# Performance work log

Hardware: AMD Instinct MI355X
Metric: run time of the kernel (lower is better)

Reference implementation:

```python
import jax, jax.numpy as jnp
import numpy as np

N_NODES = 100000
N_EDGES = 1600000
DIM = 64
BN_EPS = 1e-5


def setup_inputs() -> dict:
    key = jax.random.key(0)
    ks = jax.random.split(key, 6)
    x = jax.random.normal(ks[0], (N_NODES, DIM), dtype=jnp.float32)
    edge_index = jax.random.randint(ks[1], (2, N_EDGES), 0, N_NODES, dtype=jnp.int32)
    W = jax.random.normal(ks[2], (DIM, DIM), dtype=jnp.float32) / np.sqrt(DIM)
    b = jax.random.normal(ks[3], (DIM,), dtype=jnp.float32) * 0.01
    gamma = jnp.ones((DIM,), dtype=jnp.float32)
    beta = jnp.zeros((DIM,), dtype=jnp.float32)
    return {"x": x, "edge_index": edge_index, "W": W, "b": b, "gamma": gamma, "beta": beta}


def reference(x, edge_index, W, b, gamma, beta):
    n = x.shape[0]
    src, dst = edge_index[0], edge_index[1]
    # GCNConv adds self loops
    loop = jnp.arange(n, dtype=edge_index.dtype)
    src = jnp.concatenate([src, loop])
    dst = jnp.concatenate([dst, loop])
    # symmetric degree normalization: D^-1/2 (A+I) D^-1/2
    deg = jax.ops.segment_sum(jnp.ones(src.shape[0], x.dtype), dst, num_segments=n)
    dinv = jnp.where(deg > 0, jax.lax.rsqrt(deg), 0.0)
    norm = dinv[src] * dinv[dst]  # [E+N]
    h = x @ W  # [N, D] transform before aggregation (GCN order)
    msg = h[src] * norm[:, None]  # gather + scale
    out = jax.ops.segment_sum(msg, dst, num_segments=n) + b  # scatter-add
    # BatchNorm1d (training mode: batch statistics, biased variance)
    mean = jnp.mean(out, axis=0)
    var = jnp.mean(jnp.square(out - mean), axis=0)
    out = (out - mean) * jax.lax.rsqrt(var + BN_EPS) * gamma + beta
    # ReLU; dropout is identity in eval mode
    return jax.nn.relu(out)
```

## Files before the change

kernel.cpp:

```cpp
#include <hip/hip_runtime.h>

#define N_NODES 100000
#define N_EDGES 1600000
#define DIM 64
#define BN_EPS 1e-5f

#define BNODES 128
#define NBUCK ((N_NODES + BNODES - 1) / BNODES)
#define CAP_RAW 2560
#define CAP_OUT 3584
#define TILE 4096
#define ABLK ((N_EDGES + TILE - 1) / TILE)

#define GBLK 6250
#define NREP 32

typedef __bf16 bf16x8 __attribute__((ext_vector_type(8)));
typedef float floatx4 __attribute__((ext_vector_type(4)));

static __device__ __forceinline__ unsigned short f2bf(float f) {
    unsigned u = __float_as_uint(f);
    u = (u + 0x7FFFu + ((u >> 16) & 1u)) >> 16;
    return (unsigned short)u;
}
static __device__ __forceinline__ float bf2f(unsigned short h) {
    return __uint_as_float(((unsigned)h) << 16);
}

__global__ void __launch_bounds__(1024)
passA_kernel(const int* __restrict__ src, const int* __restrict__ dst,
             int* __restrict__ cur, unsigned int* __restrict__ entries, int E) {
    __shared__ int hist[NBUCK];
    __shared__ int lbase[NBUCK];
    int t = threadIdx.x;
    if (t < NBUCK) hist[t] = 0;
    __syncthreads();

    int e0   = blockIdx.x * TILE;
    int eend = min(e0 + TILE, E);
    int eb   = e0 + t * 4;

    int dreg[4], sreg[4], ne = 0;
    if (eb + 3 < eend) {
        int4 d4 = *(const int4*)(dst + eb);
        int4 s4 = *(const int4*)(src + eb);
        dreg[0] = d4.x; dreg[1] = d4.y; dreg[2] = d4.z; dreg[3] = d4.w;
        sreg[0] = s4.x; sreg[1] = s4.y; sreg[2] = s4.z; sreg[3] = s4.w;
        ne = 4;
    } else {
        for (int e = eb; e < eend && ne < 4; ++e, ++ne) {
            dreg[ne] = dst[e];
            sreg[ne] = src[e];
        }
    }
#pragma unroll
    for (int k = 0; k < 4; ++k)
        if (k < ne) atomicAdd(&hist[dreg[k] >> 7], 1);
    __syncthreads();
    if (t < NBUCK) {
        int ii = t + (blockIdx.x * 331) % NBUCK;
        if (ii >= NBUCK) ii -= NBUCK;
        int c = hist[ii];
        lbase[ii] = (c > 0) ? atomicAdd(&cur[ii], c) : 0;
        hist[ii] = 0;
    }
    __syncthreads();
#pragma unroll
    for (int k = 0; k < 4; ++k) {
        if (k >= ne) break;
        int s = sreg[k];
        int d = dreg[k];
        int b = d >> 7;
        int r = atomicAdd(&hist[b], 1);
        int pos = lbase[b] + r;
        if (pos < CAP_RAW)
            entries[(size_t)b * CAP_OUT + pos] = ((unsigned)s << 7) | (unsigned)(d & 127);
    }
}

__global__ void __launch_bounds__(256)
build_kernel(unsigned int* __restrict__ entries, const int* __restrict__ cur,
             int* __restrict__ rowbeg, int* __restrict__ rowend,
             float* __restrict__ dinv,
             const float* __restrict__ x, const float* __restrict__ W,
             unsigned short* __restrict__ hb, int dummyIdx, int N) {
    __shared__ int hist[BNODES * 4];
    __shared__ int nstart[BNODES];
    __shared__ int cursor[BNODES * 4];
    __shared__ float sdinv[BNODES];
    __shared__ int w0tot;
    int bucket = blockIdx.x;
    int t = threadIdx.x;
    int lane = t & 63, wv = t >> 6;
    int node0 = bucket * BNODES;
    int nn = min(BNODES, N - node0);
    int cnt = min(cur[bucket], CAP_RAW);
    unsigned int* eb = entries + (size_t)bucket * CAP_OUT;

    for (int i = t; i < BNODES * 4; i += 256) hist[i] = 0;
    __syncthreads();

    unsigned int ereg[10];
#pragma unroll
    for (int k = 0; k < 10; ++k) {
        int i = t + k * 256;
        if (i < cnt) {
            unsigned int e = eb[i];
            ereg[k] = e;
            int s = (int)(e >> 7);
            int q = (s >= 25000) + (s >= 50000) + (s >= 75000);
            atomicAdd(&hist[((e & 127) << 2) | q], 1);
        }
    }
    __syncthreads();

    int deg_t = 0, pdeg_t = 0;
    if (t < BNODES) {
        deg_t = hist[t * 4] + hist[t * 4 + 1] + hist[t * 4 + 2] + hist[t * 4 + 3];
        pdeg_t = (deg_t + 7) & ~7;
    }
    int v = pdeg_t;
#pragma unroll
    for (int off = 1; off < 64; off <<= 1) {
        int u = __shfl_up(v, off, 64);
        if (lane >= off) v += u;
    }
    if (t == 63) w0tot = v;
    __syncthreads();
    if (t < BNODES) {
        int incl = v + (wv == 1 ? w0tot : 0);
        int ex = incl - pdeg_t;
        nstart[t] = ex;
        int o = ex;
        cursor[t * 4 + 0] = o; o += hist[t * 4 + 0];
        cursor[t * 4 + 1] = o; o += hist[t * 4 + 1];
        cursor[t * 4 + 2] = o; o += hist[t * 4 + 2];
        cursor[t * 4 + 3] = o;
    }
    __syncthreads();
#pragma unroll
    for (int k = 0; k < 10; ++k) {
        int i = t + k * 256;
        if (i < cnt) {
            unsigned int e = ereg[k];
            int s = (int)(e >> 7);
            int q = (s >= 25000) + (s >= 50000) + (s >= 75000);
            int p = atomicAdd(&cursor[((e & 127) << 2) | q], 1);
            eb[p] = (unsigned)s;
        }
    }
    if (t < nn) {
        int dg  = deg_t;
        int pdg = pdeg_t;
        int base = nstart[t];
        for (int k = dg; k < pdg; ++k) eb[base + k] = (unsigned)dummyIdx;
        int gbase = bucket * CAP_OUT + base;
        rowbeg[node0 + t] = gbase;
        rowend[node0 + t] = gbase + pdg;
        float di = rsqrtf((float)(dg + 1));
        dinv[node0 + t] = di;
        sdinv[t] = di;
    }
    __syncthreads();

    int m = lane & 15, quad = lane >> 4;
    int nchunk = nn >> 4;
    bf16x8 bfrag[2][4];
#pragma unroll
    for (int c = 0; c < 2; ++c)
#pragma unroll
        for (int nt = 0; nt < 4; ++nt) {
            bf16x8 f;
#pragma unroll
            for (int j = 0; j < 8; ++j) {
                int k = c * 32 + quad * 8 + j;
                f[j] = (__bf16)W[k * DIM + nt * 16 + m];
            }
            bfrag[c][nt] = f;
        }
    for (int c2 = wv; c2 < nchunk; c2 += 4) {
        int lrow0 = c2 * 16;
        int row0 = node0 + lrow0;
        const float* xr = x + (size_t)(row0 + m) * DIM;
        bf16x8 afrag[2];
#pragma unroll
        for (int c = 0; c < 2; ++c) {
            float4 lo = *(const float4*)(xr + c * 32 + quad * 8);
            float4 hi = *(const float4*)(xr + c * 32 + quad * 8 + 4);
            bf16x8 f;
            f[0] = (__bf16)lo.x; f[1] = (__bf16)lo.y; f[2] = (__bf16)lo.z; f[3] = (__bf16)lo.w;
            f[4] = (__bf16)hi.x; f[5] = (__bf16)hi.y; f[6] = (__bf16)hi.z; f[7] = (__bf16)hi.w;
            afrag[c] = f;
        }
        float dv = sdinv[lrow0 + m];
#pragma unroll
        for (int nt = 0; nt < 4; ++nt) {
            floatx4 acc = {0.f, 0.f, 0.f, 0.f};
            acc = __builtin_amdgcn_mfma_f32_16x16x32_bf16(bfrag[0][nt], afrag[0], acc, 0, 0, 0);
            acc = __builtin_amdgcn_mfma_f32_16x16x32_bf16(bfrag[1][nt], afrag[1], acc, 0, 0, 0);
            ushort4 pk;
            pk.x = f2bf(acc[0] * dv);
            pk.y = f2bf(acc[1] * dv);
            pk.z = f2bf(acc[2] * dv);
            pk.w = f2bf(acc[3] * dv);
            *(ushort4*)(hb + (size_t)(row0 + m) * DIM + nt * 16 + quad * 4) = pk;
        }
    }
}

__global__ void __launch_bounds__(256)
gather_kernel(const int* __restrict__ rowbeg, const int* __restrict__ rowend,
              const unsigned int* __restrict__ srt, const unsigned short* __restrict__ hb,
              const float* __restrict__ dinv, unsigned short* __restrict__ hbout,
              float* __restrict__ gstatRep, int N) {
    __shared__ float red[2][4][64];
    int lane = threadIdx.x & 63;
    int wv   = threadIdx.x >> 6;
    int g    = blockIdx.x * 4 + wv;
    int n0   = g << 2;
    float s_sum = 0.f, s_sq = 0.f;

    if (n0 < N) {
        int beg = __builtin_amdgcn_readfirstlane(rowbeg[n0]);
        int s1  = __builtin_amdgcn_readfirstlane(rowbeg[n0 + 1]);
        int s2  = __builtin_amdgcn_readfirstlane(rowbeg[n0 + 2]);
        int s3  = __builtin_amdgcn_readfirstlane(rowbeg[n0 + 3]);
        int end = __builtin_amdgcn_readfirstlane(rowend[n0 + 3]);
        float acc0 = 0.f, acc1 = 0.f, acc2 = 0.f, acc3 = 0.f;

        unsigned int sv = (beg + lane < end) ? srt[beg + lane] : 0u;
        for (int base = beg; base < end; base += 64) {
            int nidx = base + 64 + lane;
            unsigned int sv_next = (nidx < end) ? srt[nidx] : 0u;
            int cn = min(64, end - base);
            int j = 0;
            for (; j + 16 <= cn; j += 16) {
                int pA = base + j;
                int pB = pA + 8;
                int kA = (pA >= s1) + (pA >= s2) + (pA >= s3);
                int kB = (pB >= s1) + (pB >= s2) + (pB >= s3);
                float v[16];
#pragma unroll
                for (int u = 0; u < 16; ++u) {
                    unsigned int s = (unsigned)__builtin_amdgcn_readlane((int)sv, j + u);
                    v[u] = bf2f(hb[(size_t)s * DIM + lane]);
                }
                float cA = ((v[0] + v[1]) + (v[2] + v[3])) +
                           ((v[4] + v[5]) + (v[6] + v[7]));
                float cB = ((v[8] + v[9]) + (v[10] + v[11])) +
                           ((v[12] + v[13]) + (v[14] + v[15]));
                acc0 += (kA == 0) ? cA : 0.f;
                acc1 += (kA == 1) ? cA : 0.f;
                acc2 += (kA == 2) ? cA : 0.f;
                acc3 += (kA == 3) ? cA : 0.f;
                acc0 += (kB == 0) ? cB : 0.f;
                acc1 += (kB == 1) ? cB : 0.f;
                acc2 += (kB == 2) ? cB : 0.f;
                acc3 += (kB == 3) ? cB : 0.f;
            }
            for (; j < cn; j += 8) {
                int p0 = base + j;
                int k = (p0 >= s1) + (p0 >= s2) + (p0 >= s3);
                float v[8];
#pragma unroll
                for (int u = 0; u < 8; ++u) {
                    unsigned int s = (unsigned)__builtin_amdgcn_readlane((int)sv, j + u);
                    v[u] = bf2f(hb[(size_t)s * DIM + lane]);
                }
                float csum = ((v[0] + v[1]) + (v[2] + v[3])) +
                             ((v[4] + v[5]) + (v[6] + v[7]));
                acc0 += (k == 0) ? csum : 0.f;
                acc1 += (k == 1) ? csum : 0.f;
                acc2 += (k == 2) ? csum : 0.f;
                acc3 += (k == 3) ? csum : 0.f;
            }
            sv = sv_next;
        }

        float v0 = (acc0 + bf2f(hb[(size_t)(n0 + 0) * DIM + lane])) * dinv[n0 + 0];
        float v1 = (acc1 + bf2f(hb[(size_t)(n0 + 1) * DIM + lane])) * dinv[n0 + 1];
        float v2 = (acc2 + bf2f(hb[(size_t)(n0 + 2) * DIM + lane])) * dinv[n0 + 2];
        float v3 = (acc3 + bf2f(hb[(size_t)(n0 + 3) * DIM + lane])) * dinv[n0 + 3];
        unsigned short r0 = f2bf(v0), r1 = f2bf(v1), r2 = f2bf(v2), r3 = f2bf(v3);
        hbout[(size_t)(n0 + 0) * DIM + lane] = r0;
        hbout[(size_t)(n0 + 1) * DIM + lane] = r1;
        hbout[(size_t)(n0 + 2) * DIM + lane] = r2;
        hbout[(size_t)(n0 + 3) * DIM + lane] = r3;
        float w0 = bf2f(r0), w1 = bf2f(r1), w2 = bf2f(r2), w3 = bf2f(r3);
        s_sum = ((w0 + w1) + (w2 + w3));
        s_sq  = ((w0 * w0 + w1 * w1) + (w2 * w2 + w3 * w3));
    }

    red[0][wv][lane] = s_sum;
    red[1][wv][lane] = s_sq;
    __syncthreads();
    if (threadIdx.x < 128) {
        int c = threadIdx.x & 63;
        int which = threadIdx.x >> 6;
        float v = red[which][0][c] + red[which][1][c] + red[which][2][c] + red[which][3][c];
        float* dst = gstatRep + (size_t)(blockIdx.x & (NREP - 1)) * 128 + which * 64 + c;
        atomicAdd(dst, v);
    }
}

__global__ void __launch_bounds__(256)
finish_kernel(const ushort4* __restrict__ hbo, float4* __restrict__ out,
              const float* __restrict__ gstatRep,
              const float* __restrict__ gamma, const float* __restrict__ beta,
              int total4, int N) {
    __shared__ float scale[64];
    __shared__ float shift[64];
    __shared__ float stat[128];
    int t = threadIdx.x;
    if (t < 128) {
        int c = t & 63;
        int which = t >> 6;
        float acc = 0.f;
#pragma unroll
        for (int r = 0; r < NREP; ++r)
            acc += gstatRep[(size_t)r * 128 + which * 64 + c];
        stat[t] = acc;
    }
    __syncthreads();
    if (t < 64) {
        float invN = 1.0f / (float)N;
        float mean = stat[t] * invN;
        float var  = stat[64 + t] * invN - mean * mean;
        float sc   = gamma[t] * rsqrtf(var + BN_EPS);
        scale[t] = sc;
        shift[t] = beta[t] - mean * sc;
    }
    __syncthreads();
    int i = blockIdx.x * blockDim.x + t;
    if (i >= total4) return;
    int c = (i * 4) & 63;
    ushort4 u = hbo[i];
    float4 v;
    float a0 = fmaf(bf2f(u.x), scale[c],     shift[c]);
    float a1 = fmaf(bf2f(u.y), scale[c + 1], shift[c + 1]);
    float a2 = fmaf(bf2f(u.z), scale[c + 2], shift[c + 2]);
    float a3 = fmaf(bf2f(u.w), scale[c + 3], shift[c + 3]);
    v.x = a0 > 0.f ? a0 : 0.f;
    v.y = a1 > 0.f ? a1 : 0.f;
    v.z = a2 > 0.f ? a2 : 0.f;
    v.w = a3 > 0.f ? a3 : 0.f;
    out[i] = v;
}

extern "C" void kernel_launch(void* const* d_in, const int* in_sizes, int n_in,
                              void* d_out, int out_size, void* d_ws, size_t ws_size,
                              hipStream_t stream) {
    const float* x     = (const float*)d_in[0];
    const int*   eidx  = (const int*)d_in[1];
    const float* W     = (const float*)d_in[2];
    const float* gamma = (const float*)d_in[4];
    const float* beta  = (const float*)d_in[5];
    float* out = (float*)d_out;

    const int N = N_NODES;
    const int total = N * DIM;

    const int* src = eidx;
    const int* dst = eidx + N_EDGES;

    char* ws = (char*)d_ws;
    size_t off_hb      = 0;
    size_t off_hbout   = off_hb + (size_t)N * DIM * 2;
    size_t off_dinv    = off_hbout + (size_t)N * DIM * 2;
    size_t off_rowbeg  = off_dinv + (size_t)N * 4;
    size_t off_rowend  = off_rowbeg + (size_t)N * 4;
    size_t off_entries = off_rowend + (size_t)N * 4;
    size_t off_z       = off_entries + (size_t)NBUCK * CAP_OUT * 4;

    unsigned short* hb     = (unsigned short*)(ws + off_hb);
    unsigned short* hbout  = (unsigned short*)(ws + off_hbout);
    float*          dinv   = (float*)(ws + off_dinv);
    int*            rowbeg = (int*)(ws + off_rowbeg);
    int*            rowend = (int*)(ws + off_rowend);
    unsigned int*   entries = (unsigned int*)(ws + off_entries);
    int*   cur      = (int*)(ws + off_z + 128);
    float* gstatRep = (float*)(cur + NBUCK);
    int dummyIdx = (int)(off_z / (DIM * 2));

    size_t zbytes = 128 + (size_t)NBUCK * 4 + (size_t)NREP * 128 * 4;
    hipMemsetAsync(ws + off_z, 0, zbytes, stream);

    passA_kernel<<<ABLK, 1024, 0, stream>>>(src, dst, cur, entries, N_EDGES);

    build_kernel<<<NBUCK, 256, 0, stream>>>(entries, cur, rowbeg, rowend, dinv,
                                            x, W, hb, dummyIdx, N);

    gather_kernel<<<GBLK, 256, 0, stream>>>(rowbeg, rowend, entries, hb, dinv,
                                            hbout, gstatRep, N);

    finish_kernel<<<(total / 4 + 255) / 256, 256, 0, stream>>>((const ushort4*)hbout,
                                                               (float4*)out, gstatRep,
                                                               gamma, beta, total / 4, N);
}
```

Baseline: 171.6 us.

## Fuse gather and BatchNorm finish into one cooperative persistent kernel

Merges the gather/aggregation kernel and the BatchNorm+ReLU finish kernel into one cooperative kernel with a persistent grid of 1024 blocks. Each wave processes up to 7 node groups, keeps the bf16 results packed in registers, does a grid-wide sync after accumulating the statistics, then applies normalization and ReLU straight from registers. This removes the bf16 intermediate write and re-read and one kernel launch. In exchange it adds a grid barrier, lowers parallelism during the gather phase, and raises register pressure.

```diff
diff --git a/kernel.cpp b/kernel.cpp
--- a/kernel.cpp
+++ b/kernel.cpp
@@ -1,4 +1,7 @@
 #include <hip/hip_runtime.h>
+#include <hip/hip_cooperative_groups.h>
+
+namespace cg = cooperative_groups;
 
 #define N_NODES 100000
 #define N_EDGES 1600000
@@ -12,8 +15,12 @@
 #define TILE 4096
 #define ABLK ((N_EDGES + TILE - 1) / TILE)
 
-#define GBLK 6250
 #define NREP 32
+
+#define CGRID 1024
+#define CWAVES (CGRID * 4)
+#define NGRP (N_NODES / 4)
+#define GPW 7
 
 typedef __bf16 bf16x8 __attribute__((ext_vector_type(8)));
 typedef float floatx4 __attribute__((ext_vector_type(4)));
@@ -208,19 +215,28 @@
     }
 }
 
-__global__ void __launch_bounds__(256)
-gather_kernel(const int* __restrict__ rowbeg, const int* __restrict__ rowend,
-              const unsigned int* __restrict__ srt, const unsigned short* __restrict__ hb,
-              const float* __restrict__ dinv, unsigned short* __restrict__ hbout,
-              float* __restrict__ gstatRep, int N) {
+__global__ void __launch_bounds__(256, 4)
+gatherbn_kernel(const int* __restrict__ rowbeg, const int* __restrict__ rowend,
+                const unsigned int* __restrict__ srt, const unsigned short* __restrict__ hb,
+                const float* __restrict__ dinv, float* __restrict__ out,
+                float* __restrict__ gstatRep,
+                const float* __restrict__ gamma, const float* __restrict__ beta) {
     __shared__ float red[2][4][64];
+    __shared__ float scale_s[64];
+    __shared__ float shift_s[64];
     int lane = threadIdx.x & 63;
     int wv   = threadIdx.x >> 6;
-    int g    = blockIdx.x * 4 + wv;
-    int n0   = g << 2;
+    int wave = blockIdx.x * 4 + wv;
     float s_sum = 0.f, s_sq = 0.f;
 
-    if (n0 < N) {
+    unsigned pk0a = 0, pk0b = 0, pk1a = 0, pk1b = 0, pk2a = 0, pk2b = 0,
+             pk3a = 0, pk3b = 0, pk4a = 0, pk4b = 0, pk5a = 0, pk5b = 0,
+             pk6a = 0, pk6b = 0;
+
+    for (int gi = 0; gi < GPW; ++gi) {
+        int g = wave + gi * CWAVES;
+        if (g >= NGRP) break;
+        int n0 = g << 2;
         int beg = __builtin_amdgcn_readfirstlane(rowbeg[n0]);
         int s1  = __builtin_amdgcn_readfirstlane(rowbeg[n0 + 1]);
         int s2  = __builtin_amdgcn_readfirstlane(rowbeg[n0 + 2]);
@@ -282,13 +298,18 @@
         float v2 = (acc2 + bf2f(hb[(size_t)(n0 + 2) * DIM + lane])) * dinv[n0 + 2];
         float v3 = (acc3 + bf2f(hb[(size_t)(n0 + 3) * DIM + lane])) * dinv[n0 + 3];
         unsigned short r0 = f2bf(v0), r1 = f2bf(v1), r2 = f2bf(v2), r3 = f2bf(v3);
-        hbout[(size_t)(n0 + 0) * DIM + lane] = r0;
-        hbout[(size_t)(n0 + 1) * DIM + lane] = r1;
-        hbout[(size_t)(n0 + 2) * DIM + lane] = r2;
-        hbout[(size_t)(n0 + 3) * DIM + lane] = r3;
+        unsigned pa = ((unsigned)r1 << 16) | (unsigned)r0;
+        unsigned pb = ((unsigned)r3 << 16) | (unsigned)r2;
+        if      (gi == 0) { pk0a = pa; pk0b = pb; }
+        else if (gi == 1) { pk1a = pa; pk1b = pb; }
+        else if (gi == 2) { pk2a = pa; pk2b = pb; }
+        else if (gi == 3) { pk3a = pa; pk3b = pb; }
+        else if (gi == 4) { pk4a = pa; pk4b = pb; }
+        else if (gi == 5) { pk5a = pa; pk5b = pb; }
+        else              { pk6a = pa; pk6b = pb; }
         float w0 = bf2f(r0), w1 = bf2f(r1), w2 = bf2f(r2), w3 = bf2f(r3);
-        s_sum = ((w0 + w1) + (w2 + w3));
-        s_sq  = ((w0 * w0 + w1 * w1) + (w2 * w2 + w3 * w3));
+        s_sum += ((w0 + w1) + (w2 + w3));
+        s_sq  += ((w0 * w0 + w1 * w1) + (w2 * w2 + w3 * w3));
     }
 
     red[0][wv][lane] = s_sum;
@@ -301,50 +322,51 @@
         float* dst = gstatRep + (size_t)(blockIdx.x & (NREP - 1)) * 128 + which * 64 + c;
         atomicAdd(dst, v);
     }
-}
-
-__global__ void __launch_bounds__(256)
-finish_kernel(const ushort4* __restrict__ hbo, float4* __restrict__ out,
-              const float* __restrict__ gstatRep,
-              const float* __restrict__ gamma, const float* __restrict__ beta,
-              int total4, int N) {
-    __shared__ float scale[64];
-    __shared__ float shift[64];
-    __shared__ float stat[128];
-    int t = threadIdx.x;
-    if (t < 128) {
-        int c = t & 63;
-        int which = t >> 6;
+    __threadfence();
+    cg::this_grid().sync();
+
+    if (threadIdx.x < 128) {
+        int c = threadIdx.x & 63;
+        int which = threadIdx.x >> 6;
         float acc = 0.f;
 #pragma unroll
         for (int r = 0; r < NREP; ++r)
             acc += gstatRep[(size_t)r * 128 + which * 64 + c];
-        stat[t] = acc;
-    }
-    __syncthreads();
-    if (t < 64) {
-        float invN = 1.0f / (float)N;
-        float mean = stat[t] * invN;
-        float var  = stat[64 + t] * invN - mean * mean;
-        float sc   = gamma[t] * rsqrtf(var + BN_EPS);
-        scale[t] = sc;
-        shift[t] = beta[t] - mean * sc;
-    }
-    __syncthreads();
-    int i = blockIdx.x * blockDim.x + t;
-    if (i >= total4) return;
-    int c = (i * 4) & 63;
-    ushort4 u = hbo[i];
-    float4 v;
-    float a0 = fmaf(bf2f(u.x), scale[c],     shift[c]);
-    float a1 = fmaf(bf2f(u.y), scale[c + 1], shift[c + 1]);
-    float a2 = fmaf(bf2f(u.z), scale[c + 2], shift[c + 2]);
-    float a3 = fmaf(bf2f(u.w), scale[c + 3], shift[c + 3]);
-    v.x = a0 > 0.f ? a0 : 0.f;
-    v.y = a1 > 0.f ? a1 : 0.f;
-    v.z = a2 > 0.f ? a2 : 0.f;
-    v.w = a3 > 0.f ? a3 : 0.f;
-    out[i] = v;
+        red[0][which][c] = acc;
+    }
+    __syncthreads();
+    if (threadIdx.x < 64) {
+        float invN = 1.0f / (float)N_NODES;
+        float mean = red[0][0][threadIdx.x] * invN;
+        float var  = red[0][1][threadIdx.x] * invN - mean * mean;
+        float sc   = gamma[threadIdx.x] * rsqrtf(var + BN_EPS);
+        scale_s[threadIdx.x] = sc;
+        shift_s[threadIdx.x] = beta[threadIdx.x] - mean * sc;
+    }
+    __syncthreads();
+
+    float sc = scale_s[lane], sh = shift_s[lane];
+    for (int gi = 0; gi < GPW; ++gi) {
+        int g = wave + gi * CWAVES;
+        if (g >= NGRP) break;
+        unsigned pa, pb;
+        if      (gi == 0) { pa = pk0a; pb = pk0b; }
+        else if (gi == 1) { pa = pk1a; pb = pk1b; }
+        else if (gi == 2) { pa = pk2a; pb = pk2b; }
+        else if (gi == 3) { pa = pk3a; pb = pk3b; }
+        else if (gi == 4) { pa = pk4a; pb = pk4b; }
+        else if (gi == 5) { pa = pk5a; pb = pk5b; }
+        else              { pa = pk6a; pb = pk6b; }
+        int n0 = g << 2;
+        float a0 = fmaf(bf2f((unsigned short)(pa & 0xFFFFu)), sc, sh);
+        float a1 = fmaf(bf2f((unsigned short)(pa >> 16)),     sc, sh);
+        float a2 = fmaf(bf2f((unsigned short)(pb & 0xFFFFu)), sc, sh);
+        float a3 = fmaf(bf2f((unsigned short)(pb >> 16)),     sc, sh);
+        out[(size_t)(n0 + 0) * DIM + lane] = a0 > 0.f ? a0 : 0.f;
+        out[(size_t)(n0 + 1) * DIM + lane] = a1 > 0.f ? a1 : 0.f;
+        out[(size_t)(n0 + 2) * DIM + lane] = a2 > 0.f ? a2 : 0.f;
+        out[(size_t)(n0 + 3) * DIM + lane] = a3 > 0.f ? a3 : 0.f;
+    }
 }
 
 extern "C" void kernel_launch(void* const* d_in, const int* in_sizes, int n_in,
@@ -358,7 +380,6 @@
     float* out = (float*)d_out;
 
     const int N = N_NODES;
-    const int total = N * DIM;
 
     const int* src = eidx;
     const int* dst = eidx + N_EDGES;
@@ -373,7 +394,6 @@
     size_t off_z       = off_entries + (size_t)NBUCK * CAP_OUT * 4;
 
     unsigned short* hb     = (unsigned short*)(ws + off_hb);
-    unsigned short* hbout  = (unsigned short*)(ws + off_hbout);
     float*          dinv   = (float*)(ws + off_dinv);
     int*            rowbeg = (int*)(ws + off_rowbeg);
     int*            rowend = (int*)(ws + off_rowend);
@@ -390,10 +410,9 @@
     build_kernel<<<NBUCK, 256, 0, stream>>>(entries, cur, rowbeg, rowend, dinv,
                                             x, W, hb, dummyIdx, N);
 
-    gather_kernel<<<GBLK, 256, 0, stream>>>(rowbeg, rowend, entries, hb, dinv,
-                                            hbout, gstatRep, N);
-
-    finish_kernel<<<(total / 4 + 255) / 256, 256, 0, stream>>>((const ushort4*)hbout,
-                                                               (float4*)out, gstatRep,
-                                                               gamma, beta, total / 4, N);
-}
+    void* kargs[] = { (void*)&rowbeg, (void*)&rowend, (void*)&entries, (void*)&hb,
+                      (void*)&dinv, (void*)&out, (void*)&gstatRep,
+                      (void*)&gamma, (void*)&beta };
+    hipLaunchCooperativeKernel((void*)gatherbn_kernel, dim3(CGRID), dim3(256),
+                               kargs, 0, stream);
+}
```

Measured after the change: 394.0 us. +129.6%, slower.

## Split GEMM out of bucket build kernel and halve passA tile size

Applied to the files above, without the earlier changes.

The dense x@W MFMA transform moves out of the per-bucket build kernel into its own gemm_kernel. That kernel launches one 256-thread block per 64 rows and reads dinv from global memory. The build kernel now only sorts edges and writes rowbeg, rowend and dinv. passA uses 2048-edge tiles with 512 threads, so twice as many blocks run with a strided loop over the histogram. The aim is more parallelism and balance in both stages, at the cost of one extra kernel launch and a dinv round trip through global memory.

```diff
diff --git a/kernel.cpp b/kernel.cpp
--- a/kernel.cpp
+++ b/kernel.cpp
@@ -9,7 +9,7 @@
 #define NBUCK ((N_NODES + BNODES - 1) / BNODES)
 #define CAP_RAW 2560
 #define CAP_OUT 3584
-#define TILE 4096
+#define TILE 2048
 #define ABLK ((N_EDGES + TILE - 1) / TILE)
 
 #define GBLK 6250
@@ -27,13 +27,13 @@
     return __uint_as_float(((unsigned)h) << 16);
 }
 
-__global__ void __launch_bounds__(1024)
+__global__ void __launch_bounds__(512)
 passA_kernel(const int* __restrict__ src, const int* __restrict__ dst,
              int* __restrict__ cur, unsigned int* __restrict__ entries, int E) {
     __shared__ int hist[NBUCK];
     __shared__ int lbase[NBUCK];
     int t = threadIdx.x;
-    if (t < NBUCK) hist[t] = 0;
+    for (int i = t; i < NBUCK; i += 512) hist[i] = 0;
     __syncthreads();
 
     int e0   = blockIdx.x * TILE;
@@ -57,8 +57,8 @@
     for (int k = 0; k < 4; ++k)
         if (k < ne) atomicAdd(&hist[dreg[k] >> 7], 1);
     __syncthreads();
-    if (t < NBUCK) {
-        int ii = t + (blockIdx.x * 331) % NBUCK;
+    for (int i = t; i < NBUCK; i += 512) {
+        int ii = i + (blockIdx.x * 331) % NBUCK;
         if (ii >= NBUCK) ii -= NBUCK;
         int c = hist[ii];
         lbase[ii] = (c > 0) ? atomicAdd(&cur[ii], c) : 0;
@@ -79,15 +79,12 @@
 }
 
 __global__ void __launch_bounds__(256)
-build_kernel(unsigned int* __restrict__ entries, const int* __restrict__ cur,
-             int* __restrict__ rowbeg, int* __restrict__ rowend,
-             float* __restrict__ dinv,
-             const float* __restrict__ x, const float* __restrict__ W,
-             unsigned short* __restrict__ hb, int dummyIdx, int N) {
+build_sort_kernel(unsigned int* __restrict__ entries, const int* __restrict__ cur,
+                  int* __restrict__ rowbeg, int* __restrict__ rowend,
+                  float* __restrict__ dinv, int dummyIdx, int N) {
     __shared__ int hist[BNODES * 4];
     __shared__ int nstart[BNODES];
     __shared__ int cursor[BNODES * 4];
-    __shared__ float sdinv[BNODES];
     __shared__ int w0tot;
     int bucket = blockIdx.x;
     int t = threadIdx.x;
@@ -157,14 +154,19 @@
         int gbase = bucket * CAP_OUT + base;
         rowbeg[node0 + t] = gbase;
         rowend[node0 + t] = gbase + pdg;
-        float di = rsqrtf((float)(dg + 1));
-        dinv[node0 + t] = di;
-        sdinv[t] = di;
-    }
-    __syncthreads();
-
+        dinv[node0 + t] = rsqrtf((float)(dg + 1));
+    }
+}
+
+__global__ void __launch_bounds__(256)
+gemm_kernel(const float* __restrict__ x, const float* __restrict__ W,
+            const float* __restrict__ dinv, unsigned short* __restrict__ hb, int N) {
+    int t = threadIdx.x;
+    int lane = t & 63, wv = t >> 6;
     int m = lane & 15, quad = lane >> 4;
-    int nchunk = nn >> 4;
+    int row0 = blockIdx.x * 64 + wv * 16;
+    if (row0 >= N) return;
+
     bf16x8 bfrag[2][4];
 #pragma unroll
     for (int c = 0; c < 2; ++c)
@@ -178,33 +180,30 @@
             }
             bfrag[c][nt] = f;
         }
-    for (int c2 = wv; c2 < nchunk; c2 += 4) {
-        int lrow0 = c2 * 16;
-        int row0 = node0 + lrow0;
-        const float* xr = x + (size_t)(row0 + m) * DIM;
-        bf16x8 afrag[2];
-#pragma unroll
-        for (int c = 0; c < 2; ++c) {
-            float4 lo = *(const float4*)(xr + c * 32 + quad * 8);
-            float4 hi = *(const float4*)(xr + c * 32 + quad * 8 + 4);
-            bf16x8 f;
-            f[0] = (__bf16)lo.x; f[1] = (__bf16)lo.y; f[2] = (__bf16)lo.z; f[3] = (__bf16)lo.w;
-            f[4] = (__bf16)hi.x; f[5] = (__bf16)hi.y; f[6] = (__bf16)hi.z; f[7] = (__bf16)hi.w;
-            afrag[c] = f;
-        }
-        float dv = sdinv[lrow0 + m];
-#pragma unroll
-        for (int nt = 0; nt < 4; ++nt) {
-            floatx4 acc = {0.f, 0.f, 0.f, 0.f};
-            acc = __builtin_amdgcn_mfma_f32_16x16x32_bf16(bfrag[0][nt], afrag[0], acc, 0, 0, 0);
-            acc = __builtin_amdgcn_mfma_f32_16x16x32_bf16(bfrag[1][nt], afrag[1], acc, 0, 0, 0);
-            ushort4 pk;
-            pk.x = f2bf(acc[0] * dv);
-            pk.y = f2bf(acc[1] * dv);
-            pk.z = f2bf(acc[2] * dv);
-            pk.w = f2bf(acc[3] * dv);
-            *(ushort4*)(hb + (size_t)(row0 + m) * DIM + nt * 16 + quad * 4) = pk;
-        }
+
+    const float* xr = x + (size_t)(row0 + m) * DIM;
+    bf16x8 afrag[2];
+#pragma unroll
+    for (int c = 0; c < 2; ++c) {
+        float4 lo = *(const float4*)(xr + c * 32 + quad * 8);
+        float4 hi = *(const float4*)(xr + c * 32 + quad * 8 + 4);
+        bf16x8 f;
+        f[0] = (__bf16)lo.x; f[1] = (__bf16)lo.y; f[2] = (__bf16)lo.z; f[3] = (__bf16)lo.w;
+        f[4] = (__bf16)hi.x; f[5] = (__bf16)hi.y; f[6] = (__bf16)hi.z; f[7] = (__bf16)hi.w;
+        afrag[c] = f;
+    }
+    float dv = dinv[row0 + m];
+#pragma unroll
+    for (int nt = 0; nt < 4; ++nt) {
+        floatx4 acc = {0.f, 0.f, 0.f, 0.f};
+        acc = __builtin_amdgcn_mfma_f32_16x16x32_bf16(bfrag[0][nt], afrag[0], acc, 0, 0, 0);
+        acc = __builtin_amdgcn_mfma_f32_16x16x32_bf16(bfrag[1][nt], afrag[1], acc, 0, 0, 0);
+        ushort4 pk;
+        pk.x = f2bf(acc[0] * dv);
+        pk.y = f2bf(acc[1] * dv);
+        pk.z = f2bf(acc[2] * dv);
+        pk.w = f2bf(acc[3] * dv);
+        *(ushort4*)(hb + (size_t)(row0 + m) * DIM + nt * 16 + quad * 4) = pk;
     }
 }
 
@@ -385,10 +384,12 @@
     size_t zbytes = 128 + (size_t)NBUCK * 4 + (size_t)NREP * 128 * 4;
     hipMemsetAsync(ws + off_z, 0, zbytes, stream);
 
-    passA_kernel<<<ABLK, 1024, 0, stream>>>(src, dst, cur, entries, N_EDGES);
-
-    build_kernel<<<NBUCK, 256, 0, stream>>>(entries, cur, rowbeg, rowend, dinv,
-                                            x, W, hb, dummyIdx, N);
+    passA_kernel<<<ABLK, 512, 0, stream>>>(src, dst, cur, entries, N_EDGES);
+
+    build_sort_kernel<<<NBUCK, 256, 0, stream>>>(entries, cur, rowbeg, rowend, dinv,
+                                                 dummyIdx, N);
+
+    gemm_kernel<<<(N + 63) / 64, 256, 0, stream>>>(x, W, dinv, hb, N);
 
     gather_kernel<<<GBLK, 256, 0, stream>>>(rowbeg, rowend, entries, hb, dinv,
                                             hbout, gstatRep, N);
```

Result: slower. 183.6 us (+7.0%).

## Prefetch x rows and W fragments early in build kernel to overlap latency

Applied to the files above, without the earlier changes.

Issues the global loads for each wave's two 16-row x tiles and the W bf16 fragments at kernel start, before the histogram and scatter phases, so their latency overlaps the atomic work. Each wave computes dinv for its rows directly from the shared histogram, which removes the sdinv shared array and one block barrier. This raises register pressure (16 float4 of x held per thread plus the W fragments) and assumes at most 8 chunks of 16 rows per bucket, which holds for BNODES=128.

```diff
diff --git a/kernel.cpp b/kernel.cpp
--- a/kernel.cpp
+++ b/kernel.cpp
@@ -87,7 +87,6 @@
     __shared__ int hist[BNODES * 4];
     __shared__ int nstart[BNODES];
     __shared__ int cursor[BNODES * 4];
-    __shared__ float sdinv[BNODES];
     __shared__ int w0tot;
     int bucket = blockIdx.x;
     int t = threadIdx.x;
@@ -97,6 +96,30 @@
     int cnt = min(cur[bucket], CAP_RAW);
     unsigned int* eb = entries + (size_t)bucket * CAP_OUT;
 
+    int m = lane & 15, quad = lane >> 4;
+    int nchunk = nn >> 4;
+    bool vA = (wv < nchunk);
+    bool vB = (wv + 4 < nchunk);
+    int rowA = node0 + wv * 16 + m;
+    int rowB = node0 + (wv + 4) * 16 + m;
+    float4 xA[4], xB[4];
+    if (vA) {
+        const float* xr = x + (size_t)rowA * DIM;
+#pragma unroll
+        for (int c = 0; c < 2; ++c) {
+            xA[c * 2]     = *(const float4*)(xr + c * 32 + quad * 8);
+            xA[c * 2 + 1] = *(const float4*)(xr + c * 32 + quad * 8 + 4);
+        }
+    }
+    if (vB) {
+        const float* xr = x + (size_t)rowB * DIM;
+#pragma unroll
+        for (int c = 0; c < 2; ++c) {
+            xB[c * 2]     = *(const float4*)(xr + c * 32 + quad * 8);
+            xB[c * 2 + 1] = *(const float4*)(xr + c * 32 + quad * 8 + 4);
+        }
+    }
+
     for (int i = t; i < BNODES * 4; i += 256) hist[i] = 0;
     __syncthreads();
 
@@ -112,7 +135,27 @@
             atomicAdd(&hist[((e & 127) << 2) | q], 1);
         }
     }
-    __syncthreads();
+
+    bf16x8 bfrag[2][4];
+#pragma unroll
+    for (int c = 0; c < 2; ++c)
+#pragma unroll
+        for (int nt = 0; nt < 4; ++nt) {
+            bf16x8 f;
+#pragma unroll
+            for (int j = 0; j < 8; ++j) {
+                int k = c * 32 + quad * 8 + j;
+                f[j] = (__bf16)W[k * DIM + nt * 16 + m];
+            }
+            bfrag[c][nt] = f;
+        }
+    __syncthreads();
+
+    int lrowA = wv * 16 + m, lrowB = (wv + 4) * 16 + m;
+    float dvA = rsqrtf((float)(1 + hist[lrowA * 4] + hist[lrowA * 4 + 1] +
+                               hist[lrowA * 4 + 2] + hist[lrowA * 4 + 3]));
+    float dvB = rsqrtf((float)(1 + hist[lrowB * 4] + hist[lrowB * 4 + 1] +
+                               hist[lrowB * 4 + 2] + hist[lrowB * 4 + 3]));
 
     int deg_t = 0, pdeg_t = 0;
     if (t < BNODES) {
@@ -157,42 +200,25 @@
         int gbase = bucket * CAP_OUT + base;
         rowbeg[node0 + t] = gbase;
         rowend[node0 + t] = gbase + pdg;
-        float di = rsqrtf((float)(dg + 1));
-        dinv[node0 + t] = di;
-        sdinv[t] = di;
-    }
-    __syncthreads();
-
-    int m = lane & 15, quad = lane >> 4;
-    int nchunk = nn >> 4;
-    bf16x8 bfrag[2][4];
-#pragma unroll
-    for (int c = 0; c < 2; ++c)
-#pragma unroll
-        for (int nt = 0; nt < 4; ++nt) {
-            bf16x8 f;
-#pragma unroll
-            for (int j = 0; j < 8; ++j) {
-                int k = c * 32 + quad * 8 + j;
-                f[j] = (__bf16)W[k * DIM + nt * 16 + m];
-            }
-            bfrag[c][nt] = f;
-        }
-    for (int c2 = wv; c2 < nchunk; c2 += 4) {
-        int lrow0 = c2 * 16;
-        int row0 = node0 + lrow0;
-        const float* xr = x + (size_t)(row0 + m) * DIM;
+        dinv[node0 + t] = rsqrtf((float)(dg + 1));
+    }
+
+#pragma unroll
+    for (int slot = 0; slot < 2; ++slot) {
+        bool valid = slot == 0 ? vA : vB;
+        if (!valid) continue;
+        int row = slot == 0 ? rowA : rowB;
+        float dv = slot == 0 ? dvA : dvB;
         bf16x8 afrag[2];
 #pragma unroll
         for (int c = 0; c < 2; ++c) {
-            float4 lo = *(const float4*)(xr + c * 32 + quad * 8);
-            float4 hi = *(const float4*)(xr + c * 32 + quad * 8 + 4);
+            float4 lo = slot == 0 ? xA[c * 2] : xB[c * 2];
+            float4 hi = slot == 0 ? xA[c * 2 + 1] : xB[c * 2 + 1];
             bf16x8 f;
             f[0] = (__bf16)lo.x; f[1] = (__bf16)lo.y; f[2] = (__bf16)lo.z; f[3] = (__bf16)lo.w;
             f[4] = (__bf16)hi.x; f[5] = (__bf16)hi.y; f[6] = (__bf16)hi.z; f[7] = (__bf16)hi.w;
             afrag[c] = f;
         }
-        float dv = sdinv[lrow0 + m];
 #pragma unroll
         for (int nt = 0; nt < 4; ++nt) {
             floatx4 acc = {0.f, 0.f, 0.f, 0.f};
@@ -203,7 +229,7 @@
             pk.y = f2bf(acc[1] * dv);
             pk.z = f2bf(acc[2] * dv);
             pk.w = f2bf(acc[3] * dv);
-            *(ushort4*)(hb + (size_t)(row0 + m) * DIM + nt * 16 + quad * 4) = pk;
+            *(ushort4*)(hb + (size_t)row * DIM + nt * 16 + quad * 4) = pk;
         }
     }
 }
```

Result: no change. 168.7 us (-1.7%).
